# Kernel tuning notes

Measured on AMD Instinct MI355X. Metric: run time of the kernel, lower is better.

Reference implementation:

```python
import jax, jax.numpy as jnp
import numpy as np

B, N, C_IN = 4, 48, 32
HID = [32, 32]          # hidden_channel_list
NB = [32, 32]           # neighborhood_channels
C_OUT = 16
N_BASIS = 6             # equivariant 2->2 basis ops used by SnConv2


def _masked(t, mask):
    # zero out entries for padded nodes; mask: B,n,n,n bool, t: B,n,n,n,C
    return jnp.where(mask[..., None], t, jnp.zeros((), t.dtype))


def snconv2(t, W, b):
    """Sn-equivariant 2nd-order conv on dims (1,2); dim 3 rides along.
    t: B,i,j,m,C.  W: [6, C_in, C_out], one mixing matrix per basis op."""
    n = t.shape[1]
    tT = jnp.swapaxes(t, 1, 2)                       # transpose op
    diag = jnp.einsum('biimc->bimc', t)              # diagonal, B,i,m,C
    rows = t.sum(axis=2) / n                         # row sums,  B,i,m,C
    cols = t.sum(axis=1) / n                         # col sums,  B,j,m,C
    tot = t.sum(axis=(1, 2)) / (n * n)               # total sum, B,m,C
    # contract small features BEFORE broadcasting back to 2nd order
    out = (jnp.einsum('bijmc,cd->bijmd', t, W[0])
           + jnp.einsum('bijmc,cd->bijmd', tT, W[1])
           + jnp.einsum('bimc,cd->bimd', diag, W[2])[:, :, None]
           + jnp.einsum('bimc,cd->bimd', rows, W[3])[:, :, None]
           + jnp.einsum('bjmc,cd->bjmd', cols, W[4])[:, None]
           + jnp.einsum('bmc,cd->bmd', tot, W[5])[:, None, None]
           + b)
    return out


def localconv2(t, Wv, bv, Ww, bw, Wo, bo):
    """LocalConv2, product_type='elementwise': per-channel message passing
    along the node dims: z[b,i,j] = sum_k v[b,i,k] * w[b,k,j] / n."""
    n = t.shape[1]
    v = jnp.einsum('bijmc,cd->bijmd', t, Wv) + bv
    w = jnp.einsum('bijmc,cd->bijmd', t, Ww) + bw
    z = jnp.einsum('bikmc,bkjmc->bijmc', v, w) / n
    return jnp.einsum('bijmc,cd->bijmd', z, Wo) + bo


def setup_inputs() -> dict:
    key = jax.random.key(0)
    ks = jax.random.split(key, 24)
    x = jax.random.normal(ks[0], (B, N, C_IN), dtype=jnp.float32)
    # graphs of unequal size: per-graph node counts in [N//2, N]
    sizes = jax.random.randint(ks[1], (B,), N // 2, N + 1)
    node_valid = jnp.arange(N)[None, :] < sizes[:, None]            # B,n
    mask = (node_valid[:, :, None, None]
            & node_valid[:, None, :, None]
            & node_valid[:, None, None, :])                          # B,n,n,n
    s = 0.05
    inp = {'x': x, 'mask': mask}
    cin = C_IN
    for li, (nch, cout) in enumerate(zip(NB, HID)):
        inp[f'basic_W{li}'] = s * jax.random.normal(ks[2 + 8 * li], (N_BASIS, cin, cin), dtype=jnp.float32)
        inp[f'basic_b{li}'] = jnp.zeros((cin,), jnp.float32)
        inp[f'lv_W{li}'] = s * jax.random.normal(ks[3 + 8 * li], (cin, nch), dtype=jnp.float32)
        inp[f'lv_b{li}'] = jnp.zeros((nch,), jnp.float32)
        inp[f'lw_W{li}'] = s * jax.random.normal(ks[4 + 8 * li], (cin, nch), dtype=jnp.float32)
        inp[f'lw_b{li}'] = jnp.zeros((nch,), jnp.float32)
        inp[f'lo_W{li}'] = s * jax.random.normal(ks[5 + 8 * li], (nch, cout), dtype=jnp.float32)
        inp[f'lo_b{li}'] = jnp.zeros((cout,), jnp.float32)
        cin = cout
    inp['final_W'] = s * jax.random.normal(ks[20], (N_BASIS, cin, C_OUT), dtype=jnp.float32)
    inp['final_b'] = jnp.zeros((C_OUT,), jnp.float32)
    return inp


def reference(x, mask,
              basic_W0, basic_b0, lv_W0, lv_b0, lw_W0, lw_b0, lo_W0, lo_b0,
              basic_W1, basic_b1, lv_W1, lv_b1, lw_W1, lw_b1, lo_W1, lo_b1,
              final_W, final_b):
    # order-3 outer product T[b,i,j,k,c] = x[b,i,c]*x[b,j,c]*x[b,k,c]
    t = (x[:, :, None, None, :] * x[:, None, :, None, :]) * x[:, None, None, :, :]
    t = _masked(t, mask)
    layers = [(basic_W0, basic_b0, lv_W0, lv_b0, lw_W0, lw_b0, lo_W0, lo_b0),
              (basic_W1, basic_b1, lv_W1, lv_b1, lw_W1, lw_b1, lo_W1, lo_b1)]
    for bw_, bb_, vw, vb, ww, wb, ow, ob in layers:
        t = _masked(snconv2(t, bw_, bb_), mask)
        t = localconv2(t, vw, vb, ww, wb, ow, ob)
        t = jax.nn.relu(t)
        t = _masked(t, mask)
    out = _masked(snconv2(t, final_W, final_b), mask)
    return out
```

## Files before the change

kernel.cpp:

```cpp
#include <hip/hip_runtime.h>
#include <cstdint>


namespace {

constexpr int nB = 4, nN = 48, nC = 32;
constexpr int SJ_ = nN * nC;
constexpr int SI_ = nN * SJ_;
constexpr long SB_ = (long)nN * SI_;
constexpr long NPOS_ = (long)nB * nN * nN * nN;

__device__ __forceinline__ void decodePos(int p, int& b, int& i, int& j, int& m) {
    m = p % nN; int r = p / nN;
    j = r % nN; r /= nN;
    i = r % nN; b = r / nN;
}

__global__ __launch_bounds__(256) void k_prep(const float* __restrict__ x,
                                              const void* __restrict__ maskp,
                                              float* __restrict__ vm,
                                              float* __restrict__ S)
{
    __shared__ float vmL[nB * nN];
    const int tid = threadIdx.x;
    const unsigned int w0 = *(const unsigned int*)maskp;
    const bool is_byte = (w0 == 0x01010101u);
    if (tid < nB * nN) {
        int b = tid / nN, i = tid % nN;
        long idx = ((long)(b * nN + i) * nN + i) * nN + i;
        int bit;
        if (is_byte) bit = (((const unsigned char*)maskp)[idx] != 0);
        else         bit = (((const int*)maskp)[idx] != 0);
        float f = bit ? 1.f : 0.f;
        vm[tid] = f; vmL[tid] = f;
    }
    __syncthreads();
    if (tid < nB * nC) {
        int b = tid >> 5, c = tid & 31;
        float s = 0.f;
        for (int j = 0; j < nN; ++j) s += x[(b * nN + j) * nC + c] * vmL[b * nN + j];
        S[tid] = s;
    }
}

__global__ __launch_bounds__(256) void k_mix0(
    const float* __restrict__ x, const float* __restrict__ S,
    const float* __restrict__ Wb, const float* __restrict__ bias,
    float* __restrict__ drp, float* __restrict__ ccp, float* __restrict__ tbp)
{
    __shared__ float W2s[1024], W3s[1024], W4s[1024], W5s[1024], bs[32];
    const int tid = threadIdx.x;
    for (int q = tid; q < 1024; q += 256) {
        W2s[q] = Wb[2048 + q]; W3s[q] = Wb[3072 + q];
        W4s[q] = Wb[4096 + q]; W5s[q] = Wb[5120 + q];
    }
    if (tid < 32) bs[tid] = bias[tid];
    __syncthreads();
    const int id = blockIdx.x * 256 + tid;
    const int m = id % nN; int r = id / nN; const int i = r % nN; const int b = r / nN;
    float odr[32], occ[32];
    #pragma unroll
    for (int d = 0; d < 32; ++d) { odr[d] = 0.f; occ[d] = 0.f; }
    for (int c2 = 0; c2 < 32; ++c2) {
        float xi = x[(b * nN + i) * nC + c2];
        float xm = x[(b * nN + m) * nC + c2];
        float sc = S[b * nC + c2];
        float A = xi * xi * xm;
        float R = xi * xm * sc * (1.f / nN);
        #pragma unroll
        for (int d = 0; d < 32; ++d) {
            odr[d] = fmaf(A, W2s[c2 * 32 + d], fmaf(R, W3s[c2 * 32 + d], odr[d]));
            occ[d] = fmaf(R, W4s[c2 * 32 + d], occ[d]);
        }
    }
    #pragma unroll
    for (int d = 0; d < 32; d += 4) {
        *(float4*)(drp + (size_t)id * 32 + d) = make_float4(odr[d], odr[d+1], odr[d+2], odr[d+3]);
        *(float4*)(ccp + (size_t)id * 32 + d) = make_float4(occ[d], occ[d+1], occ[d+2], occ[d+3]);
    }
    if (i == 0) {
        float ot[32];
        #pragma unroll
        for (int d = 0; d < 32; ++d) ot[d] = bs[d];
        for (int c2 = 0; c2 < 32; ++c2) {
            float xm = x[(b * nN + m) * nC + c2];
            float sc = S[b * nC + c2];
            float Tc = xm * sc * sc * (1.f / (nN * nN));
            #pragma unroll
            for (int d = 0; d < 32; ++d) ot[d] = fmaf(Tc, W5s[c2 * 32 + d], ot[d]);
        }
        for (int d = 0; d < 32; d += 4)
            *(float4*)(tbp + (size_t)(b * nN + m) * 32 + d) = make_float4(ot[d], ot[d+1], ot[d+2], ot[d+3]);
    }
}

template <int DOUT>
__global__ __launch_bounds__(256) void k_mix(
    const float* __restrict__ dgp, const float* __restrict__ rwp,
    const float* __restrict__ clp, const float* __restrict__ ttp,
    const float* __restrict__ Wb, const float* __restrict__ bias,
    float* __restrict__ drp, float* __restrict__ ccp, float* __restrict__ tbp)
{
    __shared__ float W2s[32 * DOUT], W3s[32 * DOUT], W4s[32 * DOUT], W5s[32 * DOUT], bs[DOUT];
    const int tid = threadIdx.x;
    for (int q = tid; q < 32 * DOUT; q += 256) {
        W2s[q] = Wb[2 * 32 * DOUT + q]; W3s[q] = Wb[3 * 32 * DOUT + q];
        W4s[q] = Wb[4 * 32 * DOUT + q]; W5s[q] = Wb[5 * 32 * DOUT + q];
    }
    if (tid < DOUT) bs[tid] = bias[tid];
    __syncthreads();
    const int id = blockIdx.x * 256 + tid;
    const int m = id % nN; int r = id / nN; const int i = r % nN; const int b = r / nN;
    float odr[DOUT], occ[DOUT];
    #pragma unroll
    for (int d = 0; d < DOUT; ++d) { odr[d] = 0.f; occ[d] = 0.f; }
    for (int c2 = 0; c2 < 32; ++c2) {
        float dg = dgp[(size_t)id * 32 + c2];
        float rw = rwp[(size_t)id * 32 + c2];
        float cl = clp[(size_t)id * 32 + c2];
        #pragma unroll
        for (int d = 0; d < DOUT; ++d) {
            odr[d] = fmaf(dg, W2s[c2 * DOUT + d], fmaf(rw, W3s[c2 * DOUT + d], odr[d]));
            occ[d] = fmaf(cl, W4s[c2 * DOUT + d], occ[d]);
        }
    }
    #pragma unroll
    for (int d = 0; d < DOUT; d += 4) {
        *(float4*)(drp + (size_t)id * DOUT + d) = make_float4(odr[d], odr[d+1], odr[d+2], odr[d+3]);
        *(float4*)(ccp + (size_t)id * DOUT + d) = make_float4(occ[d], occ[d+1], occ[d+2], occ[d+3]);
    }
    if (i == 0) {
        float ot[DOUT];
        #pragma unroll
        for (int d = 0; d < DOUT; ++d) ot[d] = bs[d];
        for (int c2 = 0; c2 < 32; ++c2) {
            float tv = ttp[(size_t)(b * nN + m) * 32 + c2];
            #pragma unroll
            for (int d = 0; d < DOUT; ++d) ot[d] = fmaf(tv, W5s[c2 * DOUT + d], ot[d]);
        }
        for (int d = 0; d < DOUT; d += 4)
            *(float4*)(tbp + (size_t)(b * nN + m) * DOUT + d) = make_float4(ot[d], ot[d+1], ot[d+2], ot[d+3]);
    }
}

__global__ __launch_bounds__(256) void k_reduce(
    const float* __restrict__ t,
    float* __restrict__ rows_, float* __restrict__ cols_,
    float* __restrict__ diag_, float* __restrict__ tot_)
{
    const int blk = blockIdx.x;
    const int iq = blk & 3; const int bm = blk >> 2;
    const int b = bm / nN, m = bm % nN;
    const int jg = threadIdx.x >> 5;
    const int c = threadIdx.x & 31;
    __shared__ float part[8][32];
    const size_t base = (size_t)b * SB_ + (size_t)m * nC;
    float colacc[6] = {0, 0, 0, 0, 0, 0};
    float totacc = 0.f;
    for (int ii = 0; ii < 12; ++ii) {
        const int i = iq * 12 + ii;
        float vals[6];
        #pragma unroll
        for (int jl = 0; jl < 6; ++jl) {
            int j = jg * 6 + jl;
            vals[jl] = t[base + (size_t)i * SI_ + (size_t)j * SJ_ + c];
        }
        float rp = 0.f;
        #pragma unroll
        for (int jl = 0; jl < 6; ++jl) { colacc[jl] += vals[jl]; rp += vals[jl]; }
        {
            int jd = i - jg * 6;
            if (jd >= 0 && jd < 6) diag_[((size_t)(b * nN + i) * nN + m) * nC + c] = vals[jd];
        }
        part[jg][c] = rp;
        __syncthreads();
        if (jg == 0) {
            float rv = 0.f;
            #pragma unroll
            for (int g = 0; g < 8; ++g) rv += part[g][c];
            rows_[((size_t)(b * nN + i) * nN + m) * nC + c] = rv * (1.f / nN);
            totacc += rv;
        }
        __syncthreads();
    }
    #pragma unroll
    for (int jl = 0; jl < 6; ++jl) {
        int j = jg * 6 + jl;
        atomicAdd(&cols_[((size_t)(b * nN + j) * nN + m) * nC + c], colacc[jl] * (1.f / nN));
    }
    if (jg == 0) atomicAdd(&tot_[(size_t)(b * nN + m) * nC + c], totacc * (1.f / (nN * nN)));
}

template <int MODE>
__global__ __launch_bounds__(256) void k_vw(
    const float* __restrict__ src, const float* __restrict__ vm,
    const float* __restrict__ drp, const float* __restrict__ ccp, const float* __restrict__ tbp,
    const float* __restrict__ W0, const float* __restrict__ W1,
    const float* __restrict__ Wv, const float* __restrict__ bv,
    const float* __restrict__ Ww, const float* __restrict__ bw,
    float* __restrict__ vout, float* __restrict__ wout)
{
    __shared__ float sA[128 * 34];
    __shared__ float sB[(MODE == 0) ? 64 : 128 * 34];
    __shared__ float sS[128 * 34];
    const int tid = threadIdx.x;
    const long base = (long)blockIdx.x * 128;

    if (MODE == 0) {
        for (int rep = 0; rep < 4; ++rep) {
            int q = rep * 256 + tid; int pl = q >> 3, cq = q & 7;
            int p = (int)base + pl;
            int b, i, j, m; decodePos(p, b, i, j, m);
            float4 xi = *(const float4*)(src + (size_t)(b * nN + i) * nC + cq * 4);
            float4 xj = *(const float4*)(src + (size_t)(b * nN + j) * nC + cq * 4);
            float4 xm = *(const float4*)(src + (size_t)(b * nN + m) * nC + cq * 4);
            int o = pl * 34 + cq * 4;
            sA[o + 0] = xi.x * xj.x * xm.x;
            sA[o + 1] = xi.y * xj.y * xm.y;
            sA[o + 2] = xi.z * xj.z * xm.z;
            sA[o + 3] = xi.w * xj.w * xm.w;
        }
    } else {
        for (int rep = 0; rep < 4; ++rep) {
            int q = rep * 256 + tid; int pl = q >> 3, cq = q & 7;
            long p = base + pl;
            float4 a = *(const float4*)(src + p * nC + cq * 4);
            int o = pl * 34 + cq * 4;
            sA[o + 0] = a.x; sA[o + 1] = a.y; sA[o + 2] = a.z; sA[o + 3] = a.w;
            int b, i, j, m; decodePos((int)p, b, i, j, m);
            long pT = ((long)(b * nN + j) * nN + i) * nN + m;
            float4 t4 = *(const float4*)(src + pT * nC + cq * 4);
            sB[o + 0] = t4.x; sB[o + 1] = t4.y; sB[o + 2] = t4.z; sB[o + 3] = t4.w;
        }
    }
    __syncthreads();

    const int pt = tid >> 3, dq = tid & 7;
    const int p0 = pt * 4, d0 = dq * 4;
    float wc[32][4];
    float acc[4][4];

    auto zeroAcc = [&]() {
        #pragma unroll
        for (int a2 = 0; a2 < 4; ++a2)
            #pragma unroll
            for (int l = 0; l < 4; ++l) acc[a2][l] = 0.f;
    };
    auto loadW = [&](const float* Wp) {
        #pragma unroll
        for (int c2 = 0; c2 < 32; ++c2) {
            float4 q4 = *(const float4*)(Wp + c2 * nC + d0);
            wc[c2][0] = q4.x; wc[c2][1] = q4.y; wc[c2][2] = q4.z; wc[c2][3] = q4.w;
        }
    };
    auto addW = [&](const float* Wp) {
        #pragma unroll
        for (int c2 = 0; c2 < 32; ++c2) {
            float4 q4 = *(const float4*)(Wp + c2 * nC + d0);
            wc[c2][0] += q4.x; wc[c2][1] += q4.y; wc[c2][2] += q4.z; wc[c2][3] += q4.w;
        }
    };
    auto sweep = [&](const float* sp) {
        #pragma unroll
        for (int c2 = 0; c2 < 32; ++c2) {
            float t0 = sp[(p0 + 0) * 34 + c2];
            float t1 = sp[(p0 + 1) * 34 + c2];
            float t2 = sp[(p0 + 2) * 34 + c2];
            float t3 = sp[(p0 + 3) * 34 + c2];
            #pragma unroll
            for (int l = 0; l < 4; ++l) {
                acc[0][l] = fmaf(t0, wc[c2][l], acc[0][l]);
                acc[1][l] = fmaf(t1, wc[c2][l], acc[1][l]);
                acc[2][l] = fmaf(t2, wc[c2][l], acc[2][l]);
                acc[3][l] = fmaf(t3, wc[c2][l], acc[3][l]);
            }
        }
    };

    zeroAcc();
    if (MODE == 0) { loadW(W0); addW(W1); sweep(sA); }
    else           { loadW(W0); sweep(sA); loadW(W1); sweep(sB); }

    #pragma unroll
    for (int l = 0; l < 4; ++l) {
        int p = (int)base + p0 + l;
        int b, i, j, m; decodePos(p, b, i, j, m);
        float4 d4 = *(const float4*)(drp + (size_t)((b * nN + i) * nN + m) * nC + d0);
        float4 c4 = *(const float4*)(ccp + (size_t)((b * nN + j) * nN + m) * nC + d0);
        float4 t4 = *(const float4*)(tbp + (size_t)(b * nN + m) * nC + d0);
        float mk = vm[b * nN + i] * vm[b * nN + j] * vm[b * nN + m];
        int o = (p0 + l) * 34 + d0;
        sS[o + 0] = (acc[l][0] + d4.x + c4.x + t4.x) * mk;
        sS[o + 1] = (acc[l][1] + d4.y + c4.y + t4.y) * mk;
        sS[o + 2] = (acc[l][2] + d4.z + c4.z + t4.z) * mk;
        sS[o + 3] = (acc[l][3] + d4.w + c4.w + t4.w) * mk;
    }
    __syncthreads();

    zeroAcc(); loadW(Wv); sweep(sS);
    {
        float4 b4 = *(const float4*)(bv + d0);
        #pragma unroll
        for (int l = 0; l < 4; ++l) {
            float4 o4 = make_float4(acc[l][0] + b4.x, acc[l][1] + b4.y,
                                    acc[l][2] + b4.z, acc[l][3] + b4.w);
            *(float4*)(vout + (size_t)(base + p0 + l) * nC + d0) = o4;
        }
    }
    zeroAcc(); loadW(Ww); sweep(sS);
    {
        float4 b4 = *(const float4*)(bw + d0);
        #pragma unroll
        for (int l = 0; l < 4; ++l) {
            float4 o4 = make_float4(acc[l][0] + b4.x, acc[l][1] + b4.y,
                                    acc[l][2] + b4.z, acc[l][3] + b4.w);
            *(float4*)(wout + (size_t)(base + p0 + l) * nC + d0) = o4;
        }
    }
}

__global__ __launch_bounds__(256) void k_z(
    const float* __restrict__ v, const float* __restrict__ w,
    const float* __restrict__ Wo, const float* __restrict__ bo,
    const float* __restrict__ vm, float* __restrict__ tout)
{
    __shared__ float lds[12416];
    const int tid = threadIdx.x;
    const int blk = blockIdx.x;
    const int tl = blk % 6; const int bm = blk / 6;
    const int it = tl >> 1, jt = tl & 1;
    const int b = bm / nN, m = bm % nN;
    const int c = tid & 31;
    const int jh = (tid >> 5) & 1;
    const int iq = tid >> 6;
    float* Vt = lds;
    float* Wt = lds + 8 * 545;
    const size_t posbase = (size_t)b * SB_ + (size_t)m * nC;
    float acc[4][12];
    #pragma unroll
    for (int l = 0; l < 4; ++l)
        #pragma unroll
        for (int u = 0; u < 12; ++u) acc[l][u] = 0.f;

    for (int kc = 0; kc < 6; ++kc) {
        __syncthreads();
        #pragma unroll
        for (int rr = 0; rr < 4; ++rr) {
            int q = rr * 256 + tid; int pos = q >> 3, cq = q & 7;
            int ii = pos >> 3, kk = pos & 7;
            int gi = it * 16 + ii, gk = kc * 8 + kk;
            float4 a = *(const float4*)(v + posbase + (size_t)gi * SI_ + (size_t)gk * SJ_ + cq * 4);
            float* dst = Vt + kk * 545 + (cq * 4) * 17 + ii;
            dst[0] = a.x; dst[17] = a.y; dst[34] = a.z; dst[51] = a.w;
        }
        #pragma unroll
        for (int rr = 0; rr < 6; ++rr) {
            int q = rr * 256 + tid; int pos = q >> 3, cq = q & 7;
            int kk = pos / 24, jj = pos % 24;
            int gk = kc * 8 + kk, gj = jt * 24 + jj;
            float4 a = *(const float4*)(w + posbase + (size_t)gk * SI_ + (size_t)gj * SJ_ + cq * 4);
            float* dst = Wt + kk * 801 + (cq * 4) * 25 + jj;
            dst[0] = a.x; dst[25] = a.y; dst[50] = a.z; dst[75] = a.w;
        }
        __syncthreads();
        #pragma unroll
        for (int kk = 0; kk < 8; ++kk) {
            float vf[4], wf[12];
            #pragma unroll
            for (int l = 0; l < 4; ++l) vf[l] = Vt[kk * 545 + c * 17 + iq * 4 + l];
            #pragma unroll
            for (int u = 0; u < 12; ++u) wf[u] = Wt[kk * 801 + c * 25 + jh * 12 + u];
            #pragma unroll
            for (int l = 0; l < 4; ++l)
                #pragma unroll
                for (int u = 0; u < 12; ++u)
                    acc[l][u] = fmaf(vf[l], wf[u], acc[l][u]);
        }
    }
    __syncthreads();
    #pragma unroll
    for (int l = 0; l < 4; ++l)
        #pragma unroll
        for (int u = 0; u < 12; ++u)
            lds[c * 388 + (iq * 4 + l) * 24 + jh * 12 + u] = acc[l][u];
    __syncthreads();

    const int pt = tid >> 3, dq = tid & 7, d0 = dq * 4;
    float wo[32][4];
    #pragma unroll
    for (int c2 = 0; c2 < 32; ++c2) {
        float4 q4 = *(const float4*)(Wo + c2 * nC + d0);
        wo[c2][0] = q4.x * (1.f / nN); wo[c2][1] = q4.y * (1.f / nN);
        wo[c2][2] = q4.z * (1.f / nN); wo[c2][3] = q4.w * (1.f / nN);
    }
    float4 b4 = *(const float4*)(bo + d0);
    float oac[12][4];
    #pragma unroll
    for (int u = 0; u < 12; ++u)
        #pragma unroll
        for (int l = 0; l < 4; ++l) oac[u][l] = 0.f;
    #pragma unroll
    for (int c2 = 0; c2 < 32; ++c2) {
        float zv[12];
        #pragma unroll
        for (int u = 0; u < 12; ++u) zv[u] = lds[c2 * 388 + pt * 12 + u];
        #pragma unroll
        for (int u = 0; u < 12; ++u)
            #pragma unroll
            for (int l = 0; l < 4; ++l)
                oac[u][l] = fmaf(zv[u], wo[c2][l], oac[u][l]);
    }
    const float vmm = vm[b * nN + m];
    #pragma unroll
    for (int u = 0; u < 12; ++u) {
        int pos = pt * 12 + u;
        int il = pos / 24, jl = pos % 24;
        int gi = it * 16 + il, gj = jt * 24 + jl;
        float mk = vm[b * nN + gi] * vm[b * nN + gj] * vmm;
        float4 o4;
        o4.x = fmaxf(oac[u][0] + b4.x, 0.f) * mk;
        o4.y = fmaxf(oac[u][1] + b4.y, 0.f) * mk;
        o4.z = fmaxf(oac[u][2] + b4.z, 0.f) * mk;
        o4.w = fmaxf(oac[u][3] + b4.w, 0.f) * mk;
        *(float4*)(tout + posbase + (size_t)gi * SI_ + (size_t)gj * SJ_ + d0) = o4;
    }
}

__global__ __launch_bounds__(256) void k_final(
    const float* __restrict__ t, const float* __restrict__ vm,
    const float* __restrict__ drp, const float* __restrict__ ccp, const float* __restrict__ tbp,
    const float* __restrict__ W0, const float* __restrict__ W1,
    float* __restrict__ out)
{
    __shared__ float sA[128 * 34], sB[128 * 34];
    const int tid = threadIdx.x;
    const long base = (long)blockIdx.x * 128;
    for (int rep = 0; rep < 4; ++rep) {
        int q = rep * 256 + tid; int pl = q >> 3, cq = q & 7;
        long p = base + pl;
        float4 a = *(const float4*)(t + p * nC + cq * 4);
        int o = pl * 34 + cq * 4;
        sA[o + 0] = a.x; sA[o + 1] = a.y; sA[o + 2] = a.z; sA[o + 3] = a.w;
        int b, i, j, m; decodePos((int)p, b, i, j, m);
        long pT = ((long)(b * nN + j) * nN + i) * nN + m;
        float4 t4 = *(const float4*)(t + pT * nC + cq * 4);
        sB[o + 0] = t4.x; sB[o + 1] = t4.y; sB[o + 2] = t4.z; sB[o + 3] = t4.w;
    }
    __syncthreads();
    const int pt = tid >> 3, dq = tid & 7;
    const int p0 = pt * 4, d0 = dq * 2;
    float wc[32][2], acc[4][2];
    #pragma unroll
    for (int l = 0; l < 4; ++l) { acc[l][0] = 0.f; acc[l][1] = 0.f; }

    #pragma unroll
    for (int c2 = 0; c2 < 32; ++c2) {
        float2 q2 = *(const float2*)(W0 + c2 * 16 + d0);
        wc[c2][0] = q2.x; wc[c2][1] = q2.y;
    }
    #pragma unroll
    for (int c2 = 0; c2 < 32; ++c2) {
        float t0 = sA[(p0 + 0) * 34 + c2], t1 = sA[(p0 + 1) * 34 + c2];
        float t2 = sA[(p0 + 2) * 34 + c2], t3 = sA[(p0 + 3) * 34 + c2];
        acc[0][0] = fmaf(t0, wc[c2][0], acc[0][0]); acc[0][1] = fmaf(t0, wc[c2][1], acc[0][1]);
        acc[1][0] = fmaf(t1, wc[c2][0], acc[1][0]); acc[1][1] = fmaf(t1, wc[c2][1], acc[1][1]);
        acc[2][0] = fmaf(t2, wc[c2][0], acc[2][0]); acc[2][1] = fmaf(t2, wc[c2][1], acc[2][1]);
        acc[3][0] = fmaf(t3, wc[c2][0], acc[3][0]); acc[3][1] = fmaf(t3, wc[c2][1], acc[3][1]);
    }
    #pragma unroll
    for (int c2 = 0; c2 < 32; ++c2) {
        float2 q2 = *(const float2*)(W1 + c2 * 16 + d0);
        wc[c2][0] = q2.x; wc[c2][1] = q2.y;
    }
    #pragma unroll
    for (int c2 = 0; c2 < 32; ++c2) {
        float t0 = sB[(p0 + 0) * 34 + c2], t1 = sB[(p0 + 1) * 34 + c2];
        float t2 = sB[(p0 + 2) * 34 + c2], t3 = sB[(p0 + 3) * 34 + c2];
        acc[0][0] = fmaf(t0, wc[c2][0], acc[0][0]); acc[0][1] = fmaf(t0, wc[c2][1], acc[0][1]);
        acc[1][0] = fmaf(t1, wc[c2][0], acc[1][0]); acc[1][1] = fmaf(t1, wc[c2][1], acc[1][1]);
        acc[2][0] = fmaf(t2, wc[c2][0], acc[2][0]); acc[2][1] = fmaf(t2, wc[c2][1], acc[2][1]);
        acc[3][0] = fmaf(t3, wc[c2][0], acc[3][0]); acc[3][1] = fmaf(t3, wc[c2][1], acc[3][1]);
    }
    #pragma unroll
    for (int l = 0; l < 4; ++l) {
        int p = (int)base + p0 + l;
        int b, i, j, m; decodePos(p, b, i, j, m);
        float2 d2 = *(const float2*)(drp + (size_t)((b * nN + i) * nN + m) * 16 + d0);
        float2 cc2 = *(const float2*)(ccp + (size_t)((b * nN + j) * nN + m) * 16 + d0);
        float2 tb2 = *(const float2*)(tbp + (size_t)(b * nN + m) * 16 + d0);
        float mk = vm[b * nN + i] * vm[b * nN + j] * vm[b * nN + m];
        float2 o2;
        o2.x = (acc[l][0] + d2.x + cc2.x + tb2.x) * mk;
        o2.y = (acc[l][1] + d2.y + cc2.y + tb2.y) * mk;
        *(float2*)(out + (size_t)p * 16 + d0) = o2;
    }
}

}

extern "C" void kernel_launch(void* const* d_in, const int* in_sizes, int n_in,
                              void* d_out, int out_size, void* d_ws, size_t ws_size,
                              hipStream_t stream)
{
    (void)in_sizes; (void)n_in; (void)out_size; (void)ws_size;
    const float* x    = (const float*)d_in[0];
    const void*  mask = d_in[1];
    const float* bW0  = (const float*)d_in[2];
    const float* bb0  = (const float*)d_in[3];
    const float* lvW0 = (const float*)d_in[4];
    const float* lvb0 = (const float*)d_in[5];
    const float* lwW0 = (const float*)d_in[6];
    const float* lwb0 = (const float*)d_in[7];
    const float* loW0 = (const float*)d_in[8];
    const float* lob0 = (const float*)d_in[9];
    const float* bW1  = (const float*)d_in[10];
    const float* bb1  = (const float*)d_in[11];
    const float* lvW1 = (const float*)d_in[12];
    const float* lvb1 = (const float*)d_in[13];
    const float* lwW1 = (const float*)d_in[14];
    const float* lwb1 = (const float*)d_in[15];
    const float* loW1 = (const float*)d_in[16];
    const float* lob1 = (const float*)d_in[17];
    const float* fW   = (const float*)d_in[18];
    const float* fb   = (const float*)d_in[19];

    float* ws  = (float*)d_ws;
    float* t   = ws;
    float* v   = ws + 14155776L;
    float* w   = ws + 28311552L;
    float* rows = ws + 42467328L;
    float* cols = rows + 294912;
    float* diag = cols + 294912;
    float* tot  = diag + 294912;
    float* dr   = tot + 6144;
    float* cc   = dr + 294912;
    float* tb   = cc + 294912;
    float* S    = tb + 6144;
    float* vm   = S + 128;
    float* out  = (float*)d_out;

    k_prep<<<1, 256, 0, stream>>>(x, mask, vm, S);
    k_mix0<<<36, 256, 0, stream>>>(x, S, bW0, bb0, dr, cc, tb);
    k_vw<0><<<3456, 256, 0, stream>>>(x, vm, dr, cc, tb, bW0, bW0 + 1024,
                                      lvW0, lvb0, lwW0, lwb0, v, w);
    k_z<<<1152, 256, 0, stream>>>(v, w, loW0, lob0, vm, t);

    hipMemsetAsync(cols, 0, 294912 * sizeof(float), stream);
    hipMemsetAsync(tot, 0, 6144 * sizeof(float), stream);
    k_reduce<<<768, 256, 0, stream>>>(t, rows, cols, diag, tot);
    k_mix<32><<<36, 256, 0, stream>>>(diag, rows, cols, tot, bW1, bb1, dr, cc, tb);
    k_vw<1><<<3456, 256, 0, stream>>>(t, vm, dr, cc, tb, bW1, bW1 + 1024,
                                      lvW1, lvb1, lwW1, lwb1, v, w);
    k_z<<<1152, 256, 0, stream>>>(v, w, loW1, lob1, vm, t);

    hipMemsetAsync(cols, 0, 294912 * sizeof(float), stream);
    hipMemsetAsync(tot, 0, 6144 * sizeof(float), stream);
    k_reduce<<<768, 256, 0, stream>>>(t, rows, cols, diag, tot);
    k_mix<16><<<36, 256, 0, stream>>>(diag, rows, cols, tot, fW, fb, dr, cc, tb);
    k_final<<<3456, 256, 0, stream>>>(t, vm, dr, cc, tb, fW, fW + 512, out);
}
```

Measured before the change: 564.1 us.

## Fuse row/col/diag/total reductions into k_z epilogue and shrink LDS footprint

Removes the separate k_reduce pass by computing row sums, column sums, diagonal and total sums inside k_z's epilogue, accumulating them with atomics, so the full t tensor is not re-read from memory. k_z's k-chunk is halved and its output is processed in two halves to cut LDS use. k_vw and k_final now reuse sA as the staging buffer, use a stride-36 layout with float4 LDS reads and a strided point mapping, and all three kernels get a launch_bounds occupancy hint of 4 blocks. In exchange there are more atomics on rows and tot, extra barriers in k_z, and possible register pressure from the occupancy hint.

```diff
diff --git a/kernel.cpp b/kernel.cpp
--- a/kernel.cpp
+++ b/kernel.cpp
@@ -8,7 +8,6 @@
 constexpr int SJ_ = nN * nC;
 constexpr int SI_ = nN * SJ_;
 constexpr long SB_ = (long)nN * SI_;
-constexpr long NPOS_ = (long)nB * nN * nN * nN;
 
 __device__ __forceinline__ void decodePos(int p, int& b, int& i, int& j, int& m) {
     m = p % nN; int r = p / nN;
@@ -143,56 +142,8 @@
     }
 }
 
-__global__ __launch_bounds__(256) void k_reduce(
-    const float* __restrict__ t,
-    float* __restrict__ rows_, float* __restrict__ cols_,
-    float* __restrict__ diag_, float* __restrict__ tot_)
-{
-    const int blk = blockIdx.x;
-    const int iq = blk & 3; const int bm = blk >> 2;
-    const int b = bm / nN, m = bm % nN;
-    const int jg = threadIdx.x >> 5;
-    const int c = threadIdx.x & 31;
-    __shared__ float part[8][32];
-    const size_t base = (size_t)b * SB_ + (size_t)m * nC;
-    float colacc[6] = {0, 0, 0, 0, 0, 0};
-    float totacc = 0.f;
-    for (int ii = 0; ii < 12; ++ii) {
-        const int i = iq * 12 + ii;
-        float vals[6];
-        #pragma unroll
-        for (int jl = 0; jl < 6; ++jl) {
-            int j = jg * 6 + jl;
-            vals[jl] = t[base + (size_t)i * SI_ + (size_t)j * SJ_ + c];
-        }
-        float rp = 0.f;
-        #pragma unroll
-        for (int jl = 0; jl < 6; ++jl) { colacc[jl] += vals[jl]; rp += vals[jl]; }
-        {
-            int jd = i - jg * 6;
-            if (jd >= 0 && jd < 6) diag_[((size_t)(b * nN + i) * nN + m) * nC + c] = vals[jd];
-        }
-        part[jg][c] = rp;
-        __syncthreads();
-        if (jg == 0) {
-            float rv = 0.f;
-            #pragma unroll
-            for (int g = 0; g < 8; ++g) rv += part[g][c];
-            rows_[((size_t)(b * nN + i) * nN + m) * nC + c] = rv * (1.f / nN);
-            totacc += rv;
-        }
-        __syncthreads();
-    }
-    #pragma unroll
-    for (int jl = 0; jl < 6; ++jl) {
-        int j = jg * 6 + jl;
-        atomicAdd(&cols_[((size_t)(b * nN + j) * nN + m) * nC + c], colacc[jl] * (1.f / nN));
-    }
-    if (jg == 0) atomicAdd(&tot_[(size_t)(b * nN + m) * nC + c], totacc * (1.f / (nN * nN)));
-}
-
 template <int MODE>
-__global__ __launch_bounds__(256) void k_vw(
+__global__ __launch_bounds__(256, 4) void k_vw(
     const float* __restrict__ src, const float* __restrict__ vm,
     const float* __restrict__ drp, const float* __restrict__ ccp, const float* __restrict__ tbp,
     const float* __restrict__ W0, const float* __restrict__ W1,
@@ -200,9 +151,8 @@
     const float* __restrict__ Ww, const float* __restrict__ bw,
     float* __restrict__ vout, float* __restrict__ wout)
 {
-    __shared__ float sA[128 * 34];
-    __shared__ float sB[(MODE == 0) ? 64 : 128 * 34];
-    __shared__ float sS[128 * 34];
+    __shared__ float sA[128 * 36];
+    __shared__ float sB[(MODE == 0) ? 4 : 128 * 36];
     const int tid = threadIdx.x;
     const long base = (long)blockIdx.x * 128;
 
@@ -214,29 +164,23 @@
             float4 xi = *(const float4*)(src + (size_t)(b * nN + i) * nC + cq * 4);
             float4 xj = *(const float4*)(src + (size_t)(b * nN + j) * nC + cq * 4);
             float4 xm = *(const float4*)(src + (size_t)(b * nN + m) * nC + cq * 4);
-            int o = pl * 34 + cq * 4;
-            sA[o + 0] = xi.x * xj.x * xm.x;
-            sA[o + 1] = xi.y * xj.y * xm.y;
-            sA[o + 2] = xi.z * xj.z * xm.z;
-            sA[o + 3] = xi.w * xj.w * xm.w;
+            *(float4*)(sA + pl * 36 + cq * 4) =
+                make_float4(xi.x * xj.x * xm.x, xi.y * xj.y * xm.y,
+                            xi.z * xj.z * xm.z, xi.w * xj.w * xm.w);
         }
     } else {
         for (int rep = 0; rep < 4; ++rep) {
             int q = rep * 256 + tid; int pl = q >> 3, cq = q & 7;
             long p = base + pl;
-            float4 a = *(const float4*)(src + p * nC + cq * 4);
-            int o = pl * 34 + cq * 4;
-            sA[o + 0] = a.x; sA[o + 1] = a.y; sA[o + 2] = a.z; sA[o + 3] = a.w;
+            *(float4*)(sA + pl * 36 + cq * 4) = *(const float4*)(src + p * nC + cq * 4);
             int b, i, j, m; decodePos((int)p, b, i, j, m);
             long pT = ((long)(b * nN + j) * nN + i) * nN + m;
-            float4 t4 = *(const float4*)(src + pT * nC + cq * 4);
-            sB[o + 0] = t4.x; sB[o + 1] = t4.y; sB[o + 2] = t4.z; sB[o + 3] = t4.w;
-        }
-    }
-    __syncthreads();
-
-    const int pt = tid >> 3, dq = tid & 7;
-    const int p0 = pt * 4, d0 = dq * 4;
+            *(float4*)(sB + pl * 36 + cq * 4) = *(const float4*)(src + pT * nC + cq * 4);
+        }
+    }
+    __syncthreads();
+
+    const int pt = tid >> 3, dq = tid & 7, d0 = dq * 4;
     float wc[32][4];
     float acc[4][4];
 
@@ -262,17 +206,26 @@
     };
     auto sweep = [&](const float* sp) {
         #pragma unroll
-        for (int c2 = 0; c2 < 32; ++c2) {
-            float t0 = sp[(p0 + 0) * 34 + c2];
-            float t1 = sp[(p0 + 1) * 34 + c2];
-            float t2 = sp[(p0 + 2) * 34 + c2];
-            float t3 = sp[(p0 + 3) * 34 + c2];
+        for (int cq2 = 0; cq2 < 8; ++cq2) {
             #pragma unroll
             for (int l = 0; l < 4; ++l) {
-                acc[0][l] = fmaf(t0, wc[c2][l], acc[0][l]);
-                acc[1][l] = fmaf(t1, wc[c2][l], acc[1][l]);
-                acc[2][l] = fmaf(t2, wc[c2][l], acc[2][l]);
-                acc[3][l] = fmaf(t3, wc[c2][l], acc[3][l]);
+                float4 tv = *(const float4*)(sp + (pt + 32 * l) * 36 + cq2 * 4);
+                acc[l][0] = fmaf(tv.x, wc[cq2*4+0][0], acc[l][0]);
+                acc[l][1] = fmaf(tv.x, wc[cq2*4+0][1], acc[l][1]);
+                acc[l][2] = fmaf(tv.x, wc[cq2*4+0][2], acc[l][2]);
+                acc[l][3] = fmaf(tv.x, wc[cq2*4+0][3], acc[l][3]);
+                acc[l][0] = fmaf(tv.y, wc[cq2*4+1][0], acc[l][0]);
+                acc[l][1] = fmaf(tv.y, wc[cq2*4+1][1], acc[l][1]);
+                acc[l][2] = fmaf(tv.y, wc[cq2*4+1][2], acc[l][2]);
+                acc[l][3] = fmaf(tv.y, wc[cq2*4+1][3], acc[l][3]);
+                acc[l][0] = fmaf(tv.z, wc[cq2*4+2][0], acc[l][0]);
+                acc[l][1] = fmaf(tv.z, wc[cq2*4+2][1], acc[l][1]);
+                acc[l][2] = fmaf(tv.z, wc[cq2*4+2][2], acc[l][2]);
+                acc[l][3] = fmaf(tv.z, wc[cq2*4+2][3], acc[l][3]);
+                acc[l][0] = fmaf(tv.w, wc[cq2*4+3][0], acc[l][0]);
+                acc[l][1] = fmaf(tv.w, wc[cq2*4+3][1], acc[l][1]);
+                acc[l][2] = fmaf(tv.w, wc[cq2*4+3][2], acc[l][2]);
+                acc[l][3] = fmaf(tv.w, wc[cq2*4+3][3], acc[l][3]);
             }
         }
     };
@@ -281,50 +234,57 @@
     if (MODE == 0) { loadW(W0); addW(W1); sweep(sA); }
     else           { loadW(W0); sweep(sA); loadW(W1); sweep(sB); }
 
+    __syncthreads();
+
     #pragma unroll
     for (int l = 0; l < 4; ++l) {
-        int p = (int)base + p0 + l;
+        int p = (int)base + pt + 32 * l;
         int b, i, j, m; decodePos(p, b, i, j, m);
         float4 d4 = *(const float4*)(drp + (size_t)((b * nN + i) * nN + m) * nC + d0);
         float4 c4 = *(const float4*)(ccp + (size_t)((b * nN + j) * nN + m) * nC + d0);
         float4 t4 = *(const float4*)(tbp + (size_t)(b * nN + m) * nC + d0);
         float mk = vm[b * nN + i] * vm[b * nN + j] * vm[b * nN + m];
-        int o = (p0 + l) * 34 + d0;
-        sS[o + 0] = (acc[l][0] + d4.x + c4.x + t4.x) * mk;
-        sS[o + 1] = (acc[l][1] + d4.y + c4.y + t4.y) * mk;
-        sS[o + 2] = (acc[l][2] + d4.z + c4.z + t4.z) * mk;
-        sS[o + 3] = (acc[l][3] + d4.w + c4.w + t4.w) * mk;
-    }
-    __syncthreads();
-
-    zeroAcc(); loadW(Wv); sweep(sS);
+        float4 s4;
+        s4.x = (acc[l][0] + d4.x + c4.x + t4.x) * mk;
+        s4.y = (acc[l][1] + d4.y + c4.y + t4.y) * mk;
+        s4.z = (acc[l][2] + d4.z + c4.z + t4.z) * mk;
+        s4.w = (acc[l][3] + d4.w + c4.w + t4.w) * mk;
+        *(float4*)(sA + (pt + 32 * l) * 36 + d0) = s4;
+    }
+    __syncthreads();
+
+    zeroAcc(); loadW(Wv); sweep(sA);
     {
         float4 b4 = *(const float4*)(bv + d0);
         #pragma unroll
         for (int l = 0; l < 4; ++l) {
             float4 o4 = make_float4(acc[l][0] + b4.x, acc[l][1] + b4.y,
                                     acc[l][2] + b4.z, acc[l][3] + b4.w);
-            *(float4*)(vout + (size_t)(base + p0 + l) * nC + d0) = o4;
-        }
-    }
-    zeroAcc(); loadW(Ww); sweep(sS);
+            *(float4*)(vout + (size_t)(base + pt + 32 * l) * nC + d0) = o4;
+        }
+    }
+    zeroAcc(); loadW(Ww); sweep(sA);
     {
         float4 b4 = *(const float4*)(bw + d0);
         #pragma unroll
         for (int l = 0; l < 4; ++l) {
             float4 o4 = make_float4(acc[l][0] + b4.x, acc[l][1] + b4.y,
                                     acc[l][2] + b4.z, acc[l][3] + b4.w);
-            *(float4*)(wout + (size_t)(base + p0 + l) * nC + d0) = o4;
-        }
-    }
-}
-
-__global__ __launch_bounds__(256) void k_z(
+            *(float4*)(wout + (size_t)(base + pt + 32 * l) * nC + d0) = o4;
+        }
+    }
+}
+
+__global__ __launch_bounds__(256, 4) void k_z(
     const float* __restrict__ v, const float* __restrict__ w,
     const float* __restrict__ Wo, const float* __restrict__ bo,
-    const float* __restrict__ vm, float* __restrict__ tout)
-{
-    __shared__ float lds[12416];
+    const float* __restrict__ vm, float* __restrict__ tout,
+    float* __restrict__ rows_, float* __restrict__ cols_,
+    float* __restrict__ diag_, float* __restrict__ tot_)
+{
+    __shared__ float lds[6208];
+    float* Vt = lds;
+    float* Wt = lds + 4 * 545;
     const int tid = threadIdx.x;
     const int blk = blockIdx.x;
     const int tl = blk % 6; const int bm = blk / 6;
@@ -333,8 +293,6 @@
     const int c = tid & 31;
     const int jh = (tid >> 5) & 1;
     const int iq = tid >> 6;
-    float* Vt = lds;
-    float* Wt = lds + 8 * 545;
     const size_t posbase = (size_t)b * SB_ + (size_t)m * nC;
     float acc[4][12];
     #pragma unroll
@@ -342,29 +300,29 @@
         #pragma unroll
         for (int u = 0; u < 12; ++u) acc[l][u] = 0.f;
 
-    for (int kc = 0; kc < 6; ++kc) {
+    for (int kc = 0; kc < 12; ++kc) {
         __syncthreads();
         #pragma unroll
-        for (int rr = 0; rr < 4; ++rr) {
+        for (int rr = 0; rr < 2; ++rr) {
             int q = rr * 256 + tid; int pos = q >> 3, cq = q & 7;
-            int ii = pos >> 3, kk = pos & 7;
-            int gi = it * 16 + ii, gk = kc * 8 + kk;
+            int ii = pos >> 2, kk = pos & 3;
+            int gi = it * 16 + ii, gk = kc * 4 + kk;
             float4 a = *(const float4*)(v + posbase + (size_t)gi * SI_ + (size_t)gk * SJ_ + cq * 4);
             float* dst = Vt + kk * 545 + (cq * 4) * 17 + ii;
             dst[0] = a.x; dst[17] = a.y; dst[34] = a.z; dst[51] = a.w;
         }
         #pragma unroll
-        for (int rr = 0; rr < 6; ++rr) {
+        for (int rr = 0; rr < 3; ++rr) {
             int q = rr * 256 + tid; int pos = q >> 3, cq = q & 7;
             int kk = pos / 24, jj = pos % 24;
-            int gk = kc * 8 + kk, gj = jt * 24 + jj;
+            int gk = kc * 4 + kk, gj = jt * 24 + jj;
             float4 a = *(const float4*)(w + posbase + (size_t)gk * SI_ + (size_t)gj * SJ_ + cq * 4);
             float* dst = Wt + kk * 801 + (cq * 4) * 25 + jj;
             dst[0] = a.x; dst[25] = a.y; dst[50] = a.z; dst[75] = a.w;
         }
         __syncthreads();
         #pragma unroll
-        for (int kk = 0; kk < 8; ++kk) {
+        for (int kk = 0; kk < 4; ++kk) {
             float vf[4], wf[12];
             #pragma unroll
             for (int l = 0; l < 4; ++l) vf[l] = Vt[kk * 545 + c * 17 + iq * 4 + l];
@@ -377,15 +335,8 @@
                     acc[l][u] = fmaf(vf[l], wf[u], acc[l][u]);
         }
     }
-    __syncthreads();
-    #pragma unroll
-    for (int l = 0; l < 4; ++l)
-        #pragma unroll
-        for (int u = 0; u < 12; ++u)
-            lds[c * 388 + (iq * 4 + l) * 24 + jh * 12 + u] = acc[l][u];
-    __syncthreads();
-
-    const int pt = tid >> 3, dq = tid & 7, d0 = dq * 4;
+
+    const int ptE = tid >> 3, dqE = tid & 7, d0 = dqE * 4;
     float wo[32][4];
     #pragma unroll
     for (int c2 = 0; c2 < 32; ++c2) {
@@ -394,96 +345,141 @@
         wo[c2][2] = q4.z * (1.f / nN); wo[c2][3] = q4.w * (1.f / nN);
     }
     float4 b4 = *(const float4*)(bo + d0);
-    float oac[12][4];
-    #pragma unroll
-    for (int u = 0; u < 12; ++u)
-        #pragma unroll
-        for (int l = 0; l < 4; ++l) oac[u][l] = 0.f;
-    #pragma unroll
-    for (int c2 = 0; c2 < 32; ++c2) {
-        float zv[12];
-        #pragma unroll
-        for (int u = 0; u < 12; ++u) zv[u] = lds[c2 * 388 + pt * 12 + u];
-        #pragma unroll
-        for (int u = 0; u < 12; ++u)
+    const float vmm = vm[b * nN + m];
+
+    for (int h = 0; h < 2; ++h) {
+        __syncthreads();
+        if ((iq >> 1) == h) {
+            int il0 = (iq & 1) * 4;
             #pragma unroll
             for (int l = 0; l < 4; ++l)
-                oac[u][l] = fmaf(zv[u], wo[c2][l], oac[u][l]);
-    }
-    const float vmm = vm[b * nN + m];
-    #pragma unroll
-    for (int u = 0; u < 12; ++u) {
-        int pos = pt * 12 + u;
-        int il = pos / 24, jl = pos % 24;
-        int gi = it * 16 + il, gj = jt * 24 + jl;
-        float mk = vm[b * nN + gi] * vm[b * nN + gj] * vmm;
-        float4 o4;
-        o4.x = fmaxf(oac[u][0] + b4.x, 0.f) * mk;
-        o4.y = fmaxf(oac[u][1] + b4.y, 0.f) * mk;
-        o4.z = fmaxf(oac[u][2] + b4.z, 0.f) * mk;
-        o4.w = fmaxf(oac[u][3] + b4.w, 0.f) * mk;
-        *(float4*)(tout + posbase + (size_t)gi * SI_ + (size_t)gj * SJ_ + d0) = o4;
-    }
-}
-
-__global__ __launch_bounds__(256) void k_final(
+                #pragma unroll
+                for (int u = 0; u < 12; ++u)
+                    lds[c * 194 + (il0 + l) * 24 + jh * 12 + u] = acc[l][u];
+        }
+        __syncthreads();
+
+        float outv[6][4];
+        {
+            float oac[6][4];
+            #pragma unroll
+            for (int u = 0; u < 6; ++u)
+                #pragma unroll
+                for (int l = 0; l < 4; ++l) oac[u][l] = 0.f;
+            #pragma unroll
+            for (int c2 = 0; c2 < 32; ++c2) {
+                float zv[6];
+                #pragma unroll
+                for (int u = 0; u < 6; ++u) zv[u] = lds[c2 * 194 + ptE * 6 + u];
+                #pragma unroll
+                for (int u = 0; u < 6; ++u)
+                    #pragma unroll
+                    for (int l = 0; l < 4; ++l)
+                        oac[u][l] = fmaf(zv[u], wo[c2][l], oac[u][l]);
+            }
+            #pragma unroll
+            for (int u = 0; u < 6; ++u) {
+                int q = ptE * 6 + u;
+                int il = q / 24, jl = q % 24;
+                int gi = it * 16 + 8 * h + il, gj = jt * 24 + jl;
+                float mk = vm[b * nN + gi] * vm[b * nN + gj] * vmm;
+                float4 o4;
+                o4.x = fmaxf(oac[u][0] + b4.x, 0.f) * mk;
+                o4.y = fmaxf(oac[u][1] + b4.y, 0.f) * mk;
+                o4.z = fmaxf(oac[u][2] + b4.z, 0.f) * mk;
+                o4.w = fmaxf(oac[u][3] + b4.w, 0.f) * mk;
+                outv[u][0] = o4.x; outv[u][1] = o4.y; outv[u][2] = o4.z; outv[u][3] = o4.w;
+                *(float4*)(tout + posbase + (size_t)gi * SI_ + (size_t)gj * SJ_ + d0) = o4;
+            }
+        }
+        __syncthreads();
+        #pragma unroll
+        for (int l = 0; l < 4; ++l)
+            #pragma unroll
+            for (int u = 0; u < 6; ++u)
+                lds[(d0 + l) * 194 + ptE * 6 + u] = outv[u][l];
+        __syncthreads();
+
+        {
+            int il_r = tid >> 5, c_r = tid & 31;
+            float rsum = 0.f;
+            #pragma unroll
+            for (int jl = 0; jl < 24; ++jl) rsum += lds[c_r * 194 + il_r * 24 + jl];
+            int gi_r = it * 16 + 8 * h + il_r;
+            atomicAdd(&rows_[((size_t)(b * nN + gi_r) * nN + m) * nC + c_r], rsum * (1.f / nN));
+            atomicAdd(&tot_[(size_t)(b * nN + m) * nC + c_r], rsum * (1.f / (nN * nN)));
+            int jl_d = gi_r - jt * 24;
+            if (jl_d >= 0 && jl_d < 24)
+                diag_[((size_t)(b * nN + gi_r) * nN + m) * nC + c_r] =
+                    lds[c_r * 194 + il_r * 24 + jl_d];
+        }
+        #pragma unroll
+        for (int rr = 0; rr < 3; ++rr) {
+            int task = rr * 256 + tid;
+            int c_c = task & 31, jl_c = task >> 5;
+            float csum = 0.f;
+            #pragma unroll
+            for (int il = 0; il < 8; ++il) csum += lds[c_c * 194 + il * 24 + jl_c];
+            atomicAdd(&cols_[((size_t)(b * nN + (jt * 24 + jl_c)) * nN + m) * nC + c_c],
+                      csum * (1.f / nN));
+        }
+    }
+}
+
+__global__ __launch_bounds__(256, 4) void k_final(
     const float* __restrict__ t, const float* __restrict__ vm,
     const float* __restrict__ drp, const float* __restrict__ ccp, const float* __restrict__ tbp,
     const float* __restrict__ W0, const float* __restrict__ W1,
     float* __restrict__ out)
 {
-    __shared__ float sA[128 * 34], sB[128 * 34];
+    __shared__ float sA[128 * 36], sB[128 * 36];
     const int tid = threadIdx.x;
     const long base = (long)blockIdx.x * 128;
     for (int rep = 0; rep < 4; ++rep) {
         int q = rep * 256 + tid; int pl = q >> 3, cq = q & 7;
         long p = base + pl;
-        float4 a = *(const float4*)(t + p * nC + cq * 4);
-        int o = pl * 34 + cq * 4;
-        sA[o + 0] = a.x; sA[o + 1] = a.y; sA[o + 2] = a.z; sA[o + 3] = a.w;
+        *(float4*)(sA + pl * 36 + cq * 4) = *(const float4*)(t + p * nC + cq * 4);
         int b, i, j, m; decodePos((int)p, b, i, j, m);
         long pT = ((long)(b * nN + j) * nN + i) * nN + m;
-        float4 t4 = *(const float4*)(t + pT * nC + cq * 4);
-        sB[o + 0] = t4.x; sB[o + 1] = t4.y; sB[o + 2] = t4.z; sB[o + 3] = t4.w;
-    }
-    __syncthreads();
-    const int pt = tid >> 3, dq = tid & 7;
-    const int p0 = pt * 4, d0 = dq * 2;
+        *(float4*)(sB + pl * 36 + cq * 4) = *(const float4*)(t + pT * nC + cq * 4);
+    }
+    __syncthreads();
+    const int pt = tid >> 3, dq = tid & 7, d0 = dq * 2;
     float wc[32][2], acc[4][2];
     #pragma unroll
     for (int l = 0; l < 4; ++l) { acc[l][0] = 0.f; acc[l][1] = 0.f; }
 
-    #pragma unroll
-    for (int c2 = 0; c2 < 32; ++c2) {
-        float2 q2 = *(const float2*)(W0 + c2 * 16 + d0);
-        wc[c2][0] = q2.x; wc[c2][1] = q2.y;
-    }
-    #pragma unroll
-    for (int c2 = 0; c2 < 32; ++c2) {
-        float t0 = sA[(p0 + 0) * 34 + c2], t1 = sA[(p0 + 1) * 34 + c2];
-        float t2 = sA[(p0 + 2) * 34 + c2], t3 = sA[(p0 + 3) * 34 + c2];
-        acc[0][0] = fmaf(t0, wc[c2][0], acc[0][0]); acc[0][1] = fmaf(t0, wc[c2][1], acc[0][1]);
-        acc[1][0] = fmaf(t1, wc[c2][0], acc[1][0]); acc[1][1] = fmaf(t1, wc[c2][1], acc[1][1]);
-        acc[2][0] = fmaf(t2, wc[c2][0], acc[2][0]); acc[2][1] = fmaf(t2, wc[c2][1], acc[2][1]);
-        acc[3][0] = fmaf(t3, wc[c2][0], acc[3][0]); acc[3][1] = fmaf(t3, wc[c2][1], acc[3][1]);
-    }
-    #pragma unroll
-    for (int c2 = 0; c2 < 32; ++c2) {
-        float2 q2 = *(const float2*)(W1 + c2 * 16 + d0);
-        wc[c2][0] = q2.x; wc[c2][1] = q2.y;
-    }
-    #pragma unroll
-    for (int c2 = 0; c2 < 32; ++c2) {
-        float t0 = sB[(p0 + 0) * 34 + c2], t1 = sB[(p0 + 1) * 34 + c2];
-        float t2 = sB[(p0 + 2) * 34 + c2], t3 = sB[(p0 + 3) * 34 + c2];
-        acc[0][0] = fmaf(t0, wc[c2][0], acc[0][0]); acc[0][1] = fmaf(t0, wc[c2][1], acc[0][1]);
-        acc[1][0] = fmaf(t1, wc[c2][0], acc[1][0]); acc[1][1] = fmaf(t1, wc[c2][1], acc[1][1]);
-        acc[2][0] = fmaf(t2, wc[c2][0], acc[2][0]); acc[2][1] = fmaf(t2, wc[c2][1], acc[2][1]);
-        acc[3][0] = fmaf(t3, wc[c2][0], acc[3][0]); acc[3][1] = fmaf(t3, wc[c2][1], acc[3][1]);
-    }
+    auto loadW = [&](const float* Wp) {
+        #pragma unroll
+        for (int c2 = 0; c2 < 32; ++c2) {
+            float2 q2 = *(const float2*)(Wp + c2 * 16 + d0);
+            wc[c2][0] = q2.x; wc[c2][1] = q2.y;
+        }
+    };
+    auto sweep = [&](const float* sp) {
+        #pragma unroll
+        for (int cq2 = 0; cq2 < 8; ++cq2) {
+            #pragma unroll
+            for (int l = 0; l < 4; ++l) {
+                float4 tv = *(const float4*)(sp + (pt + 32 * l) * 36 + cq2 * 4);
+                acc[l][0] = fmaf(tv.x, wc[cq2*4+0][0], acc[l][0]);
+                acc[l][1] = fmaf(tv.x, wc[cq2*4+0][1], acc[l][1]);
+                acc[l][0] = fmaf(tv.y, wc[cq2*4+1][0], acc[l][0]);
+                acc[l][1] = fmaf(tv.y, wc[cq2*4+1][1], acc[l][1]);
+                acc[l][0] = fmaf(tv.z, wc[cq2*4+2][0], acc[l][0]);
+                acc[l][1] = fmaf(tv.z, wc[cq2*4+2][1], acc[l][1]);
+                acc[l][0] = fmaf(tv.w, wc[cq2*4+3][0], acc[l][0]);
+                acc[l][1] = fmaf(tv.w, wc[cq2*4+3][1], acc[l][1]);
+            }
+        }
+    };
+
+    loadW(W0); sweep(sA);
+    loadW(W1); sweep(sB);
+
     #pragma unroll
     for (int l = 0; l < 4; ++l) {
-        int p = (int)base + p0 + l;
+        int p = (int)base + pt + 32 * l;
         int b, i, j, m; decodePos(p, b, i, j, m);
         float2 d2 = *(const float2*)(drp + (size_t)((b * nN + i) * nN + m) * 16 + d0);
         float2 cc2 = *(const float2*)(ccp + (size_t)((b * nN + j) * nN + m) * 16 + d0);
@@ -543,19 +539,16 @@
     k_mix0<<<36, 256, 0, stream>>>(x, S, bW0, bb0, dr, cc, tb);
     k_vw<0><<<3456, 256, 0, stream>>>(x, vm, dr, cc, tb, bW0, bW0 + 1024,
                                       lvW0, lvb0, lwW0, lwb0, v, w);
-    k_z<<<1152, 256, 0, stream>>>(v, w, loW0, lob0, vm, t);
-
-    hipMemsetAsync(cols, 0, 294912 * sizeof(float), stream);
+    hipMemsetAsync(rows, 0, 2 * 294912 * sizeof(float), stream);
     hipMemsetAsync(tot, 0, 6144 * sizeof(float), stream);
-    k_reduce<<<768, 256, 0, stream>>>(t, rows, cols, diag, tot);
+    k_z<<<1152, 256, 0, stream>>>(v, w, loW0, lob0, vm, t, rows, cols, diag, tot);
     k_mix<32><<<36, 256, 0, stream>>>(diag, rows, cols, tot, bW1, bb1, dr, cc, tb);
+
     k_vw<1><<<3456, 256, 0, stream>>>(t, vm, dr, cc, tb, bW1, bW1 + 1024,
                                       lvW1, lvb1, lwW1, lwb1, v, w);
-    k_z<<<1152, 256, 0, stream>>>(v, w, loW1, lob1, vm, t);
-
-    hipMemsetAsync(cols, 0, 294912 * sizeof(float), stream);
+    hipMemsetAsync(rows, 0, 2 * 294912 * sizeof(float), stream);
     hipMemsetAsync(tot, 0, 6144 * sizeof(float), stream);
-    k_reduce<<<768, 256, 0, stream>>>(t, rows, cols, diag, tot);
+    k_z<<<1152, 256, 0, stream>>>(v, w, loW1, lob1, vm, t, rows, cols, diag, tot);
     k_mix<16><<<36, 256, 0, stream>>>(diag, rows, cols, tot, fW, fb, dr, cc, tb);
     k_final<<<3456, 256, 0, stream>>>(t, vm, dr, cc, tb, fW, fW + 512, out);
 }
```

Result: slower. 759.3 us (+34.6%).
